# Performance work log

Measured on AMD Instinct MI355X. Metric: run time of the kernel, lower is better.

The kernel has to match this reference:

```python
import jax, jax.numpy as jnp
import numpy as np

N_NODE = 100000
DEPTH = 10
N_EDGE = 1600000
D_FEAT = 32
BASE_ALPHA = 1.0


def setup_inputs() -> dict:
    key = jax.random.key(0)
    k1, k2 = jax.random.split(key)
    x = jax.random.normal(k1, (N_NODE, D_FEAT), dtype=jnp.float32)
    edge_index = jax.random.randint(k2, (2, N_EDGE), 0, N_NODE, dtype=jnp.int64)
    edge_attr = jnp.ones((N_EDGE,), dtype=jnp.float32)
    # alphas init: min(1/alpha, 1) = 1.0 for each of depth+1 coefficients
    alphas = jnp.ones((DEPTH + 1,), dtype=jnp.float32)
    return {"x": x, "edge_index": edge_index, "edge_attr": edge_attr, "alphas": alphas}


def reference(x, edge_index, edge_attr, alphas):
    n_node = x.shape[0]
    row, col = edge_index[0], edge_index[1]

    # GCN normalization: val = deg^-1/2[row] * w * deg^-1/2[col]
    deg = jax.ops.segment_sum(jnp.ones_like(edge_attr), row, num_segments=n_node)
    deg = jnp.where(deg < 0.5, deg + 1.0, deg)
    dinv = deg ** -0.5
    val = dinv[row] * edge_attr * dinv[col]  # (E,)

    def adj_mul(h):  # sparse A @ h via gather + segment_sum (coalesce-equivalent)
        return jax.ops.segment_sum(val[:, None] * h[col], row, num_segments=n_node)

    alphas_t = BASE_ALPHA * jnp.tanh(alphas)  # (depth+1,)

    # PowerConv (monomial basis): x_0 = x; x_L = alpha_L * (A @ x_{L-1})
    xs = [x]
    for L in range(1, DEPTH + 1):
        xs.append(alphas_t[L] * adj_mul(xs[-1]))
    return jnp.stack(xs, axis=1)  # (n_node, depth+1, d_feat)
```

## Files before the change

kernel.cpp:

```cpp
#include <hip/hip_runtime.h>
#include <math.h>

#define N_NODE 100000
#define DEPTH  10
#define N_EDGE 1600000
#define D_FEAT 32
#define D_OUT  ((DEPTH + 1) * D_FEAT)
#define NB_SCAN ((N_NODE + 255) / 256)
#define SPMM_BLOCKS 2048

typedef float        f32x4 __attribute__((ext_vector_type(4)));
typedef unsigned int u32x4 __attribute__((ext_vector_type(4)));
typedef int          i32x2 __attribute__((ext_vector_type(2)));

__device__ inline unsigned short f32_to_bf16(float f) {
    unsigned int b = __float_as_uint(f);
    unsigned int r = (b + 0x7FFFu + ((b >> 16) & 1u)) >> 16;
    return (unsigned short)r;
}
__device__ inline unsigned int pack_bf16x2(float lo, float hi) {
    return (unsigned int)f32_to_bf16(lo) | ((unsigned int)f32_to_bf16(hi) << 16);
}

__global__ void count_kernel(const int* __restrict__ row, int* __restrict__ cnt, int E) {
    int e = blockIdx.x * blockDim.x + threadIdx.x;
    if (e < E) atomicAdd(&cnt[row[e]], 1);
}

__device__ inline int wave_incl_scan(int v) {
    int lane = threadIdx.x & 63;
    #pragma unroll
    for (int off = 1; off < 64; off <<= 1) {
        int t = __shfl_up(v, off, 64);
        if (lane >= off) v += t;
    }
    return v;
}

__global__ void blockscan_kernel(const int* __restrict__ cnt, int* __restrict__ rowStart,
                                 int* __restrict__ blockSums, int n) {
    __shared__ int partials[4];
    int i = blockIdx.x * 256 + threadIdx.x;
    int v = (i < n) ? cnt[i] : 0;
    int incl = wave_incl_scan(v);
    int wid = threadIdx.x >> 6, lane = threadIdx.x & 63;
    if (lane == 63) partials[wid] = incl;
    __syncthreads();
    int woff = 0;
    #pragma unroll
    for (int w = 0; w < 4; ++w) woff += (w < wid) ? partials[w] : 0;
    if (i < n) rowStart[i] = woff + incl - v;
    if (threadIdx.x == 255) blockSums[blockIdx.x] = woff + incl;
}

__global__ void scansums_kernel(int* __restrict__ blockSums, int nb) {
    __shared__ int partials[8];
    int i = threadIdx.x;
    int v = (i < nb) ? blockSums[i] : 0;
    int incl = wave_incl_scan(v);
    int wid = i >> 6, lane = i & 63;
    if (lane == 63) partials[wid] = incl;
    __syncthreads();
    int woff = 0;
    #pragma unroll
    for (int w = 0; w < 8; ++w) woff += (w < wid) ? partials[w] : 0;
    if (i < nb) blockSums[i] = woff + incl - v;
    if (i == 511) blockSums[nb] = woff + incl;
}

__global__ void addoffs_kernel(int* __restrict__ rowStart, const int* __restrict__ blockSums,
                               int n, int nb) {
    int i = blockIdx.x * 256 + threadIdx.x;
    if (i < n)  rowStart[i] += blockSums[i >> 8];
    if (i == n) rowStart[n] = blockSums[nb];
}

__global__ void dinv_kernel(const int* __restrict__ cnt, float* __restrict__ dinv, int n) {
    int i = blockIdx.x * blockDim.x + threadIdx.x;
    if (i < n) {
        float d = (float)cnt[i];
        if (d < 0.5f) d += 1.0f;
        dinv[i] = 1.0f / sqrtf(d);
    }
}

__global__ void scatter_kernel(const int* __restrict__ row, const int* __restrict__ col,
                               const float* __restrict__ eattr,
                               const int* __restrict__ rowStart, int* __restrict__ cnt,
                               const float* __restrict__ dinv,
                               i32x2* __restrict__ csr, int E) {
    int e = blockIdx.x * blockDim.x + threadIdx.x;
    if (e < E) {
        int r = row[e], c = col[e];
        int p = rowStart[r] + atomicSub(&cnt[r], 1) - 1;
        float val = dinv[r] * eattr[e] * dinv[c];
        i32x2 ent; ent.x = c; ent.y = __float_as_int(val);
        __builtin_nontemporal_store(ent, &csr[p]);
    }
}

__global__ void alpha_kernel(const float* __restrict__ alphas, float* __restrict__ alphaT) {
    int i = threadIdx.x;
    if (i <= DEPTH) alphaT[i] = tanhf(alphas[i]);
}

__global__ void copyx_kernel(const f32x4* __restrict__ x4, f32x4* __restrict__ out4,
                             unsigned int* __restrict__ h0) {
    int i = blockIdx.x * blockDim.x + threadIdx.x;
    if (i < N_NODE * 8) {
        int node = i >> 3, q = i & 7;
        f32x4 v = x4[i];
        __builtin_nontemporal_store(v, &out4[(size_t)node * 88 + q]);
        h0[i * 2]     = pack_bf16x2(v.x, v.y);
        h0[i * 2 + 1] = pack_bf16x2(v.z, v.w);
    }
}

__global__ __launch_bounds__(256) void spmm_kernel(const int* __restrict__ rowStart,
                                                   const i32x2* __restrict__ csr,
                                                   const float* __restrict__ alphaT,
                                                   int L,
                                                   const u32x4* __restrict__ h_prev,
                                                   u32x4* __restrict__ h_cur,
                                                   f32x4* __restrict__ out4) {
    int lane = threadIdx.x & 63;
    int s = lane >> 2;
    int q = lane & 3;
    float a = alphaT[L];

    int wave   = (int)((blockIdx.x * 256 + threadIdx.x) >> 6);
    int nwaves = SPMM_BLOCKS * 4;

    for (int rowid = wave; rowid < N_NODE; rowid += nwaves) {
        int start = rowStart[rowid];
        int end   = rowStart[rowid + 1];

        float acc[8] = {0.f, 0.f, 0.f, 0.f, 0.f, 0.f, 0.f, 0.f};
        for (int e = start + s; e < end; e += 16) {
            i32x2 cv = __builtin_nontemporal_load(&csr[e]);
            float v  = __int_as_float(cv.y);
            u32x4 h  = h_prev[(size_t)cv.x * 4 + q];
            acc[0] += v * __uint_as_float(h.x << 16);
            acc[1] += v * __uint_as_float(h.x & 0xFFFF0000u);
            acc[2] += v * __uint_as_float(h.y << 16);
            acc[3] += v * __uint_as_float(h.y & 0xFFFF0000u);
            acc[4] += v * __uint_as_float(h.z << 16);
            acc[5] += v * __uint_as_float(h.z & 0xFFFF0000u);
            acc[6] += v * __uint_as_float(h.w << 16);
            acc[7] += v * __uint_as_float(h.w & 0xFFFF0000u);
        }

        #pragma unroll
        for (int m = 4; m < 64; m <<= 1) {
            #pragma unroll
            for (int k = 0; k < 8; ++k) acc[k] += __shfl_xor(acc[k], m, 64);
        }

        if (s == 0) {
            #pragma unroll
            for (int k = 0; k < 8; ++k) acc[k] *= a;
            size_t ob = (size_t)rowid * 88 + L * 8 + q * 2;
            f32x4 o0; o0.x = acc[0]; o0.y = acc[1]; o0.z = acc[2]; o0.w = acc[3];
            f32x4 o1; o1.x = acc[4]; o1.y = acc[5]; o1.z = acc[6]; o1.w = acc[7];
            __builtin_nontemporal_store(o0, &out4[ob]);
            __builtin_nontemporal_store(o1, &out4[ob + 1]);
            if (L < DEPTH) {
                u32x4 hh;
                hh.x = pack_bf16x2(acc[0], acc[1]);
                hh.y = pack_bf16x2(acc[2], acc[3]);
                hh.z = pack_bf16x2(acc[4], acc[5]);
                hh.w = pack_bf16x2(acc[6], acc[7]);
                h_cur[(size_t)rowid * 4 + q] = hh;
            }
        }
    }
}

extern "C" void kernel_launch(void* const* d_in, const int* in_sizes, int n_in,
                              void* d_out, int out_size, void* d_ws, size_t ws_size,
                              hipStream_t stream) {
    const float* x      = (const float*)d_in[0];
    const int*   eidx   = (const int*)d_in[1];
    const float* eattr  = (const float*)d_in[2];
    const float* alphas = (const float*)d_in[3];
    float* out = (float*)d_out;

    const int* row = eidx;
    const int* col = eidx + N_EDGE;

    char* p = (char*)d_ws;
    auto alloc = [&](size_t bytes) { char* r = p; p += (bytes + 255) & ~(size_t)255; return (void*)r; };
    int*   cnt       = (int*)  alloc((size_t)N_NODE * 4);
    int*   rowStart  = (int*)  alloc((size_t)(N_NODE + 1) * 4);
    int*   blockSums = (int*)  alloc((size_t)(NB_SCAN + 1) * 4);
    float* dinv      = (float*)alloc((size_t)N_NODE * 4);
    float* alphaT    = (float*)alloc(64);
    u32x4* h0        = (u32x4*)alloc((size_t)N_NODE * 64);
    u32x4* h1        = (u32x4*)alloc((size_t)N_NODE * 64);
    i32x2* csr       = (i32x2*)alloc((size_t)N_EDGE * 8);
    (void)ws_size; (void)in_sizes; (void)n_in; (void)out_size;

    (void)hipMemsetAsync(cnt, 0, (size_t)N_NODE * 4, stream);

    const int TB = 256;
    int eBlocks = (N_EDGE + TB - 1) / TB;
    int nBlocks = (N_NODE + TB - 1) / TB;

    count_kernel<<<eBlocks, TB, 0, stream>>>(row, cnt, N_EDGE);
    blockscan_kernel<<<NB_SCAN, TB, 0, stream>>>(cnt, rowStart, blockSums, N_NODE);
    scansums_kernel<<<1, 512, 0, stream>>>(blockSums, NB_SCAN);
    addoffs_kernel<<<(N_NODE + 1 + TB - 1) / TB, TB, 0, stream>>>(rowStart, blockSums, N_NODE, NB_SCAN);
    dinv_kernel<<<nBlocks, TB, 0, stream>>>(cnt, dinv, N_NODE);
    scatter_kernel<<<eBlocks, TB, 0, stream>>>(row, col, eattr, rowStart, cnt, dinv, csr, N_EDGE);
    alpha_kernel<<<1, 64, 0, stream>>>(alphas, alphaT);
    copyx_kernel<<<(N_NODE * 8 + TB - 1) / TB, TB, 0, stream>>>((const f32x4*)x, (f32x4*)out,
                                                                (unsigned int*)h0);

    for (int L = 1; L <= DEPTH; ++L) {
        const u32x4* hp = (L & 1) ? h0 : h1;
        u32x4*       hc = (L & 1) ? h1 : h0;
        spmm_kernel<<<SPMM_BLOCKS, TB, 0, stream>>>(rowStart, csr, alphaT, L, hp, hc,
                                                    (f32x4*)out);
    }
}
```

Measured before the change: 609.7 us.

## Fuse all propagation layers into one persistent kernel with grid barrier

Replaces the ten per-layer SpMM launches with a single persistent kernel of 768 blocks that loops over layers and synchronizes with a software grid-wide atomic barrier. The goal is to remove kernel launch gaps and tail drain between layers. This relies on all 768 blocks being co-resident, since the barrier would deadlock otherwise. The smaller grid may also expose less memory parallelism per layer.

```diff
diff --git a/kernel.cpp b/kernel.cpp
--- a/kernel.cpp
+++ b/kernel.cpp
@@ -7,7 +7,7 @@
 #define D_FEAT 32
 #define D_OUT  ((DEPTH + 1) * D_FEAT)
 #define NB_SCAN ((N_NODE + 255) / 256)
-#define SPMM_BLOCKS 2048
+#define SPMM_BLOCKS 768
 
 typedef float        f32x4 __attribute__((ext_vector_type(4)));
 typedef unsigned int u32x4 __attribute__((ext_vector_type(4)));
@@ -116,62 +116,79 @@
     }
 }
 
-__global__ __launch_bounds__(256) void spmm_kernel(const int* __restrict__ rowStart,
-                                                   const i32x2* __restrict__ csr,
-                                                   const float* __restrict__ alphaT,
-                                                   int L,
-                                                   const u32x4* __restrict__ h_prev,
-                                                   u32x4* __restrict__ h_cur,
-                                                   f32x4* __restrict__ out4) {
+__global__ __launch_bounds__(256, 4) void spmm_fused(const int* __restrict__ rowStart,
+                                                     const i32x2* __restrict__ csr,
+                                                     const float* __restrict__ alphaT,
+                                                     u32x4* __restrict__ h0,
+                                                     u32x4* __restrict__ h1,
+                                                     f32x4* __restrict__ out4,
+                                                     int* __restrict__ bar) {
     int lane = threadIdx.x & 63;
     int s = lane >> 2;
     int q = lane & 3;
-    float a = alphaT[L];
-
     int wave   = (int)((blockIdx.x * 256 + threadIdx.x) >> 6);
-    int nwaves = SPMM_BLOCKS * 4;
-
-    for (int rowid = wave; rowid < N_NODE; rowid += nwaves) {
-        int start = rowStart[rowid];
-        int end   = rowStart[rowid + 1];
-
-        float acc[8] = {0.f, 0.f, 0.f, 0.f, 0.f, 0.f, 0.f, 0.f};
-        for (int e = start + s; e < end; e += 16) {
-            i32x2 cv = __builtin_nontemporal_load(&csr[e]);
-            float v  = __int_as_float(cv.y);
-            u32x4 h  = h_prev[(size_t)cv.x * 4 + q];
-            acc[0] += v * __uint_as_float(h.x << 16);
-            acc[1] += v * __uint_as_float(h.x & 0xFFFF0000u);
-            acc[2] += v * __uint_as_float(h.y << 16);
-            acc[3] += v * __uint_as_float(h.y & 0xFFFF0000u);
-            acc[4] += v * __uint_as_float(h.z << 16);
-            acc[5] += v * __uint_as_float(h.z & 0xFFFF0000u);
-            acc[6] += v * __uint_as_float(h.w << 16);
-            acc[7] += v * __uint_as_float(h.w & 0xFFFF0000u);
+    const int nwaves = SPMM_BLOCKS * 4;
+
+    for (int L = 1; L <= DEPTH; ++L) {
+        const u32x4* __restrict__ hp = (L & 1) ? h0 : h1;
+        u32x4*       __restrict__ hc = (L & 1) ? h1 : h0;
+        float a = alphaT[L];
+
+        for (int rowid = wave; rowid < N_NODE; rowid += nwaves) {
+            int start = rowStart[rowid];
+            int end   = rowStart[rowid + 1];
+
+            float acc[8] = {0.f, 0.f, 0.f, 0.f, 0.f, 0.f, 0.f, 0.f};
+            for (int e = start + s; e < end; e += 16) {
+                i32x2 cv = __builtin_nontemporal_load(&csr[e]);
+                float v  = __int_as_float(cv.y);
+                u32x4 h  = hp[(size_t)cv.x * 4 + q];
+                acc[0] += v * __uint_as_float(h.x << 16);
+                acc[1] += v * __uint_as_float(h.x & 0xFFFF0000u);
+                acc[2] += v * __uint_as_float(h.y << 16);
+                acc[3] += v * __uint_as_float(h.y & 0xFFFF0000u);
+                acc[4] += v * __uint_as_float(h.z << 16);
+                acc[5] += v * __uint_as_float(h.z & 0xFFFF0000u);
+                acc[6] += v * __uint_as_float(h.w << 16);
+                acc[7] += v * __uint_as_float(h.w & 0xFFFF0000u);
+            }
+
+            #pragma unroll
+            for (int m = 4; m < 64; m <<= 1) {
+                #pragma unroll
+                for (int k = 0; k < 8; ++k) acc[k] += __shfl_xor(acc[k], m, 64);
+            }
+
+            if (s == 0) {
+                #pragma unroll
+                for (int k = 0; k < 8; ++k) acc[k] *= a;
+                size_t ob = (size_t)rowid * 88 + L * 8 + q * 2;
+                f32x4 o0; o0.x = acc[0]; o0.y = acc[1]; o0.z = acc[2]; o0.w = acc[3];
+                f32x4 o1; o1.x = acc[4]; o1.y = acc[5]; o1.z = acc[6]; o1.w = acc[7];
+                __builtin_nontemporal_store(o0, &out4[ob]);
+                __builtin_nontemporal_store(o1, &out4[ob + 1]);
+                if (L < DEPTH) {
+                    u32x4 hh;
+                    hh.x = pack_bf16x2(acc[0], acc[1]);
+                    hh.y = pack_bf16x2(acc[2], acc[3]);
+                    hh.z = pack_bf16x2(acc[4], acc[5]);
+                    hh.w = pack_bf16x2(acc[6], acc[7]);
+                    hc[(size_t)rowid * 4 + q] = hh;
+                }
+            }
         }
 
-        #pragma unroll
-        for (int m = 4; m < 64; m <<= 1) {
-            #pragma unroll
-            for (int k = 0; k < 8; ++k) acc[k] += __shfl_xor(acc[k], m, 64);
-        }
-
-        if (s == 0) {
-            #pragma unroll
-            for (int k = 0; k < 8; ++k) acc[k] *= a;
-            size_t ob = (size_t)rowid * 88 + L * 8 + q * 2;
-            f32x4 o0; o0.x = acc[0]; o0.y = acc[1]; o0.z = acc[2]; o0.w = acc[3];
-            f32x4 o1; o1.x = acc[4]; o1.y = acc[5]; o1.z = acc[6]; o1.w = acc[7];
-            __builtin_nontemporal_store(o0, &out4[ob]);
-            __builtin_nontemporal_store(o1, &out4[ob + 1]);
-            if (L < DEPTH) {
-                u32x4 hh;
-                hh.x = pack_bf16x2(acc[0], acc[1]);
-                hh.y = pack_bf16x2(acc[2], acc[3]);
-                hh.z = pack_bf16x2(acc[4], acc[5]);
-                hh.w = pack_bf16x2(acc[6], acc[7]);
-                h_cur[(size_t)rowid * 4 + q] = hh;
-            }
+        if (L < DEPTH) {
+            __syncthreads();
+            if (threadIdx.x == 0) {
+                __threadfence();
+                __hip_atomic_fetch_add(bar, 1, __ATOMIC_RELEASE, __HIP_MEMORY_SCOPE_AGENT);
+                int target = SPMM_BLOCKS * L;
+                while (__hip_atomic_load(bar, __ATOMIC_ACQUIRE, __HIP_MEMORY_SCOPE_AGENT) < target) {
+                    __builtin_amdgcn_s_sleep(8);
+                }
+            }
+            __syncthreads();
         }
     }
 }
@@ -195,12 +212,14 @@
     int*   blockSums = (int*)  alloc((size_t)(NB_SCAN + 1) * 4);
     float* dinv      = (float*)alloc((size_t)N_NODE * 4);
     float* alphaT    = (float*)alloc(64);
+    int*   bar       = (int*)  alloc(256);
     u32x4* h0        = (u32x4*)alloc((size_t)N_NODE * 64);
     u32x4* h1        = (u32x4*)alloc((size_t)N_NODE * 64);
     i32x2* csr       = (i32x2*)alloc((size_t)N_EDGE * 8);
     (void)ws_size; (void)in_sizes; (void)n_in; (void)out_size;
 
     (void)hipMemsetAsync(cnt, 0, (size_t)N_NODE * 4, stream);
+    (void)hipMemsetAsync(bar, 0, 4, stream);
 
     const int TB = 256;
     int eBlocks = (N_EDGE + TB - 1) / TB;
@@ -216,10 +235,6 @@
     copyx_kernel<<<(N_NODE * 8 + TB - 1) / TB, TB, 0, stream>>>((const f32x4*)x, (f32x4*)out,
                                                                 (unsigned int*)h0);
 
-    for (int L = 1; L <= DEPTH; ++L) {
-        const u32x4* hp = (L & 1) ? h0 : h1;
-        u32x4*       hc = (L & 1) ? h1 : h0;
-        spmm_kernel<<<SPMM_BLOCKS, TB, 0, stream>>>(rowStart, csr, alphaT, L, hp, hc,
-                                                    (f32x4*)out);
-    }
-}
+    spmm_fused<<<SPMM_BLOCKS, TB, 0, stream>>>(rowStart, csr, alphaT, h0, h1,
+                                               (f32x4*)out, bar);
+}
```

After: 1.929 ms. +216.4%, slower.

## Process four rows per wave in SpMM to overlap gathers across rows

Applied to the files above, without the earlier changes.

Replaces the grid-stride one-row-per-wave SpMM with a kernel in which each wave handles four consecutive rows. It issues the CSR and feature-gather loads for all four rows before accumulating, so more memory requests are in flight. Lanes past a row's end are clamped and masked to zero, and the launch now covers every node exactly. The cost is four times the accumulator registers, with lanes idling while the longest of the four rows finishes.

```diff
diff --git a/kernel.cpp b/kernel.cpp
--- a/kernel.cpp
+++ b/kernel.cpp
@@ -7,7 +7,6 @@
 #define D_FEAT 32
 #define D_OUT  ((DEPTH + 1) * D_FEAT)
 #define NB_SCAN ((N_NODE + 255) / 256)
-#define SPMM_BLOCKS 2048
 
 typedef float        f32x4 __attribute__((ext_vector_type(4)));
 typedef unsigned int u32x4 __attribute__((ext_vector_type(4)));
@@ -111,66 +110,93 @@
         int node = i >> 3, q = i & 7;
         f32x4 v = x4[i];
         __builtin_nontemporal_store(v, &out4[(size_t)node * 88 + q]);
-        h0[i * 2]     = pack_bf16x2(v.x, v.y);
-        h0[i * 2 + 1] = pack_bf16x2(v.z, v.w);
-    }
-}
-
-__global__ __launch_bounds__(256) void spmm_kernel(const int* __restrict__ rowStart,
-                                                   const i32x2* __restrict__ csr,
-                                                   const float* __restrict__ alphaT,
-                                                   int L,
-                                                   const u32x4* __restrict__ h_prev,
-                                                   u32x4* __restrict__ h_cur,
-                                                   f32x4* __restrict__ out4) {
+        h0[(size_t)node * 16 + q * 2]     = pack_bf16x2(v.x, v.y);
+        h0[(size_t)node * 16 + q * 2 + 1] = pack_bf16x2(v.z, v.w);
+    }
+}
+
+__global__ __launch_bounds__(256) void spmm_quad(const int* __restrict__ rowStart,
+                                                 const i32x2* __restrict__ csr,
+                                                 const float* __restrict__ alphaT,
+                                                 int L,
+                                                 const u32x4* __restrict__ h_prev,
+                                                 u32x4* __restrict__ h_cur,
+                                                 f32x4* __restrict__ out4) {
+    int wave = (int)((blockIdx.x * 256 + threadIdx.x) >> 6);
     int lane = threadIdx.x & 63;
     int s = lane >> 2;
     int q = lane & 3;
-    float a = alphaT[L];
-
-    int wave   = (int)((blockIdx.x * 256 + threadIdx.x) >> 6);
-    int nwaves = SPMM_BLOCKS * 4;
-
-    for (int rowid = wave; rowid < N_NODE; rowid += nwaves) {
-        int start = rowStart[rowid];
-        int end   = rowStart[rowid + 1];
-
-        float acc[8] = {0.f, 0.f, 0.f, 0.f, 0.f, 0.f, 0.f, 0.f};
-        for (int e = start + s; e < end; e += 16) {
-            i32x2 cv = __builtin_nontemporal_load(&csr[e]);
-            float v  = __int_as_float(cv.y);
-            u32x4 h  = h_prev[(size_t)cv.x * 4 + q];
-            acc[0] += v * __uint_as_float(h.x << 16);
-            acc[1] += v * __uint_as_float(h.x & 0xFFFF0000u);
-            acc[2] += v * __uint_as_float(h.y << 16);
-            acc[3] += v * __uint_as_float(h.y & 0xFFFF0000u);
-            acc[4] += v * __uint_as_float(h.z << 16);
-            acc[5] += v * __uint_as_float(h.z & 0xFFFF0000u);
-            acc[6] += v * __uint_as_float(h.w << 16);
-            acc[7] += v * __uint_as_float(h.w & 0xFFFF0000u);
-        }
-
-        #pragma unroll
-        for (int m = 4; m < 64; m <<= 1) {
+    int base = wave * 4;
+
+    int rs[5];
+    #pragma unroll
+    for (int i = 0; i < 5; ++i) rs[i] = rowStart[base + i];
+
+    int be[4], en[4];
+    #pragma unroll
+    for (int r = 0; r < 4; ++r) { be[r] = rs[r]; en[r] = rs[r + 1]; }
+
+    float acc[4][8];
+    #pragma unroll
+    for (int r = 0; r < 4; ++r)
+        #pragma unroll
+        for (int k = 0; k < 8; ++k) acc[r][k] = 0.f;
+
+    while ((be[0] < en[0]) | (be[1] < en[1]) | (be[2] < en[2]) | (be[3] < en[3])) {
+        i32x2 cv[4];
+        #pragma unroll
+        for (int r = 0; r < 4; ++r) {
+            int e  = be[r] + s;
+            int ec = (e < N_EDGE - 1) ? e : (N_EDGE - 1);
+            cv[r] = __builtin_nontemporal_load(&csr[ec]);
+        }
+        u32x4 hv[4];
+        #pragma unroll
+        for (int r = 0; r < 4; ++r) {
+            hv[r] = h_prev[(size_t)cv[r].x * 4 + q];
+        }
+        #pragma unroll
+        for (int r = 0; r < 4; ++r) {
+            float v = (be[r] + s < en[r]) ? __int_as_float(cv[r].y) : 0.f;
+            u32x4 h = hv[r];
+            acc[r][0] += v * __uint_as_float(h.x << 16);
+            acc[r][1] += v * __uint_as_float(h.x & 0xFFFF0000u);
+            acc[r][2] += v * __uint_as_float(h.y << 16);
+            acc[r][3] += v * __uint_as_float(h.y & 0xFFFF0000u);
+            acc[r][4] += v * __uint_as_float(h.z << 16);
+            acc[r][5] += v * __uint_as_float(h.z & 0xFFFF0000u);
+            acc[r][6] += v * __uint_as_float(h.w << 16);
+            acc[r][7] += v * __uint_as_float(h.w & 0xFFFF0000u);
+        }
+        #pragma unroll
+        for (int r = 0; r < 4; ++r) be[r] += 16;
+    }
+
+    #pragma unroll
+    for (int r = 0; r < 4; ++r)
+        #pragma unroll
+        for (int m = 4; m < 64; m <<= 1)
             #pragma unroll
-            for (int k = 0; k < 8; ++k) acc[k] += __shfl_xor(acc[k], m, 64);
-        }
-
-        if (s == 0) {
+            for (int k = 0; k < 8; ++k) acc[r][k] += __shfl_xor(acc[r][k], m, 64);
+
+    if (s == 0) {
+        float a = alphaT[L];
+        #pragma unroll
+        for (int r = 0; r < 4; ++r) {
             #pragma unroll
-            for (int k = 0; k < 8; ++k) acc[k] *= a;
-            size_t ob = (size_t)rowid * 88 + L * 8 + q * 2;
-            f32x4 o0; o0.x = acc[0]; o0.y = acc[1]; o0.z = acc[2]; o0.w = acc[3];
-            f32x4 o1; o1.x = acc[4]; o1.y = acc[5]; o1.z = acc[6]; o1.w = acc[7];
+            for (int k = 0; k < 8; ++k) acc[r][k] *= a;
+            size_t ob = (size_t)(base + r) * 88 + L * 8 + q * 2;
+            f32x4 o0; o0.x = acc[r][0]; o0.y = acc[r][1]; o0.z = acc[r][2]; o0.w = acc[r][3];
+            f32x4 o1; o1.x = acc[r][4]; o1.y = acc[r][5]; o1.z = acc[r][6]; o1.w = acc[r][7];
             __builtin_nontemporal_store(o0, &out4[ob]);
             __builtin_nontemporal_store(o1, &out4[ob + 1]);
             if (L < DEPTH) {
                 u32x4 hh;
-                hh.x = pack_bf16x2(acc[0], acc[1]);
-                hh.y = pack_bf16x2(acc[2], acc[3]);
-                hh.z = pack_bf16x2(acc[4], acc[5]);
-                hh.w = pack_bf16x2(acc[6], acc[7]);
-                h_cur[(size_t)rowid * 4 + q] = hh;
+                hh.x = pack_bf16x2(acc[r][0], acc[r][1]);
+                hh.y = pack_bf16x2(acc[r][2], acc[r][3]);
+                hh.z = pack_bf16x2(acc[r][4], acc[r][5]);
+                hh.w = pack_bf16x2(acc[r][6], acc[r][7]);
+                h_cur[(size_t)(base + r) * 4 + q] = hh;
             }
         }
     }
@@ -191,7 +217,7 @@
     char* p = (char*)d_ws;
     auto alloc = [&](size_t bytes) { char* r = p; p += (bytes + 255) & ~(size_t)255; return (void*)r; };
     int*   cnt       = (int*)  alloc((size_t)N_NODE * 4);
-    int*   rowStart  = (int*)  alloc((size_t)(N_NODE + 1) * 4);
+    int*   rowStart  = (int*)  alloc((size_t)(N_NODE + 8) * 4);
     int*   blockSums = (int*)  alloc((size_t)(NB_SCAN + 1) * 4);
     float* dinv      = (float*)alloc((size_t)N_NODE * 4);
     float* alphaT    = (float*)alloc(64);
@@ -216,10 +242,11 @@
     copyx_kernel<<<(N_NODE * 8 + TB - 1) / TB, TB, 0, stream>>>((const f32x4*)x, (f32x4*)out,
                                                                 (unsigned int*)h0);
 
+    int quadBlocks = N_NODE / 4 / 4;
     for (int L = 1; L <= DEPTH; ++L) {
         const u32x4* hp = (L & 1) ? h0 : h1;
         u32x4*       hc = (L & 1) ? h1 : h0;
-        spmm_kernel<<<SPMM_BLOCKS, TB, 0, stream>>>(rowStart, csr, alphaT, L, hp, hc,
-                                                    (f32x4*)out);
-    }
-}
+        spmm_quad<<<quadBlocks, TB, 0, stream>>>(rowStart, csr, alphaT, L, hp, hc,
+                                                 (f32x4*)out);
+    }
+}
```

Result: faster. 566.1 us (-7.2%).
